# Kernel tuning notes

Hardware: AMD Instinct MI355X
Metric: run time of the kernel (lower is better)

## Reference

```python
import jax, jax.numpy as jnp
from jax import lax
import numpy as np

SEL = [46, 92]
A_SEL = [16, 32]
EPS = 1e-16


def _descriptors(xyz, atomtypes, box):
    # xyz: (B,N,3) float, atomtypes: (B,N) int, box: scalar
    B, N, _ = xyz.shape
    dm = xyz[:, :, None, :] - xyz[:, None, :, :] + EPS          # (B,N,N,3)
    dm = dm - box * jnp.round(dm / box)                          # min-image PBC
    dist = jnp.sqrt(jnp.sum(dm * dm, axis=-1))                   # (B,N,N)
    self_mask = jnp.eye(N, dtype=bool)[None]                     # exclude self
    radial, a_xyz_list, a_dist_list = [], [], []
    lf_d = lf_i = None
    for j, (selj, aselj) in enumerate(zip(SEL, A_SEL)):
        mask = (atomtypes == j)[:, None, :] & (~self_mask)       # (B,N,N)
        d_j = jnp.where(mask, dist, jnp.inf)
        k = max(selj, aselj, 2)
        neg, idx = lax.top_k(-d_j, k)                            # k smallest
        sd = -neg                                                # (B,N,k)
        if j == 0:
            lf_d, lf_i = sd[..., :2], idx[..., :2]
        else:
            better = sd[..., :2] < lf_d
            lf_d = jnp.where(better, sd[..., :2], lf_d)
            lf_i = jnp.where(better, idx[..., :2], lf_i)
        radial.append(1.0 / (sd[..., :selj] + EPS))
        a_xyz_list.append(jnp.take_along_axis(dm, idx[..., :aselj, None], axis=2))
        a_dist_list.append(sd[..., :aselj])
    a_xyz = jnp.concatenate(a_xyz_list, axis=2)                  # (B,N,sumA,3)
    a_dist = jnp.concatenate(a_dist_list, axis=2)[..., None]     # (B,N,sumA,1)
    # local frame from the 2 globally nearest neighbors
    l_xyz = jnp.take_along_axis(dm, lf_i[..., None], axis=2) / (lf_d[..., None] + EPS)
    r0, r1 = l_xyz[:, :, 0], l_xyz[:, :, 1]                      # (B,N,3)
    v2 = r1 - jnp.sum(r0 * r1, -1, keepdims=True) * r0
    v2 = v2 / jnp.linalg.norm(v2, axis=-1, keepdims=True)
    v3 = jnp.cross(r0, r1)
    v3 = v3 / jnp.linalg.norm(v3, axis=-1, keepdims=True)
    A = jnp.stack([r0, v2, v3], axis=-2)                         # (B,N,3,3)
    a_xyz = a_xyz / (a_dist + EPS)
    a_xyz = jnp.einsum('bnij,bnkj->bnki', A, a_xyz)
    a_xyz = a_xyz / (a_dist + EPS)  # faithful: source divides by a_dist twice
    return jnp.concatenate(radial + [a_xyz.reshape(B, N, -1)], axis=-1)


def _energy(xyz, atomtypes, box, params):
    # norm is (mean=0, std=1) in the source -> identity, skipped.
    desc = _descriptors(xyz, atomtypes, box)
    e = jnp.zeros(desc.shape[:2], desc.dtype)
    for t, layers in enumerate(params):
        h = desc
        for (W, b) in layers[:-1]:
            h = jnp.tanh(h @ W + b)
        W, b = layers[-1]
        e = jnp.where(atomtypes == t, (h @ W + b)[..., 0], e)
    return jnp.sum(e, axis=1)                                    # (B,)


def setup_inputs():
    key = jax.random.key(0)
    ks = jax.random.split(key, 16)
    B, N, box = 2, 2048, 27
    xyz = jax.random.uniform(ks[0], (B, N, 3), dtype=jnp.float32) * box
    atomtypes = jax.random.randint(ks[1], (B, N), 0, 2)
    D = sum(SEL) + 3 * sum(A_SEL)  # 282
    sizes = [D, 64, 64, 1]
    inp = {'xyz': xyz, 'atomtypes': atomtypes, 'box_size': box}
    ki = 2
    for t in range(2):
        for l in range(3):
            fi, fo = sizes[l], sizes[l + 1]
            inp[f'W{t}_{l}'] = jax.random.normal(ks[ki], (fi, fo), dtype=jnp.float32) / np.sqrt(fi).astype(np.float32)
            inp[f'b{t}_{l}'] = jnp.zeros((fo,), jnp.float32)
            ki += 1
    return inp


def reference(xyz, atomtypes, box_size, W0_0, b0_0, W0_1, b0_1, W0_2, b0_2,
              W1_0, b1_0, W1_1, b1_1, W1_2, b1_2):
    params = [[(W0_0, b0_0), (W0_1, b0_1), (W0_2, b0_2)],
              [(W1_0, b1_0), (W1_1, b1_1), (W1_2, b1_2)]]
    energy = _energy(xyz, atomtypes, box_size, params)
    forces = -jax.grad(lambda x: jnp.sum(_energy(x, atomtypes, box_size, params)))(xyz)
    return energy, forces
```

## Files before the change

kernel.cpp:

```cpp
#include <hip/hip_runtime.h>
#include <stdint.h>
#include <math.h>

#define BLOCK 256
#define WPB 4
#define SEL0 46
#define SEL1 92
#define ASEL0 16
#define ASEL1 32
#define NNB 138
#define NANG 48
#define DDIM 282
#define HID 64
#define FEPS 1e-16f
#define NPT 32
#define CAP 128
#define NMAX 2048
#define SFE (3*NMAX)
#define RGROUPS 8

__device__ __forceinline__ float mimg(float dx, float box, float ibox) {
    return dx - box * rintf(dx * ibox);
}

__device__ __forceinline__ void wsync() {
    asm volatile("s_waitcnt lgkmcnt(0)" ::: "memory");
    __builtin_amdgcn_wave_barrier();
}

__device__ __forceinline__ void decode(unsigned long long k, float& d, int& j) {
    uint32_t idx = (uint32_t)(k & 0xFFFFFFFFull);
    if (idx == 0xFFFFFFFFu) { d = 1e30f; j = -1; }
    else { d = __uint_as_float((uint32_t)(k >> 32)); j = (int)idx; }
}

__global__ __launch_bounds__(BLOCK)
void reduce_kernel(const float* __restrict__ rep, float* __restrict__ out,
                   int total, int B, int N, int sstride, int nspb, int rgs)
{
    int e = blockIdx.x * BLOCK + threadIdx.x;
    if (e >= total) return;
    int r0 = blockIdx.y * rgs;
    if (r0 >= nspb) return;
    int r1 = min(r0 + rgs, nspb);
    const float* p;
    if (e < B) {
        p = rep + (size_t)e * nspb * sstride + 3 * N;
    } else {
        int f = e - B;
        int b = f / (3 * N);
        int elem = f - b * 3 * N;
        p = rep + (size_t)b * nspb * sstride + elem;
    }
    p += (size_t)r0 * sstride;
    float s0=0,s1=0,s2=0,s3=0,s4=0,s5=0,s6=0,s7=0;
    int r = r0;
    const size_t st = (size_t)sstride;
    for (; r + 8 <= r1; r += 8) {
        s0 += p[0*st]; s1 += p[1*st]; s2 += p[2*st]; s3 += p[3*st];
        s4 += p[4*st]; s5 += p[5*st]; s6 += p[6*st]; s7 += p[7*st];
        p += 8*st;
    }
    float s = ((s0+s1)+(s2+s3)) + ((s4+s5)+(s6+s7));
    for (; r < r1; ++r) { s += *p; p += st; }
    atomicAdd(&out[e], s);
}

__global__ __launch_bounds__(BLOCK, 2)
void md_kernel(const float* __restrict__ xyz, const int* __restrict__ types,
               const void* __restrict__ boxp,
               const float* __restrict__ W0a, const float* __restrict__ B0a,
               const float* __restrict__ W1a, const float* __restrict__ B1a,
               const float* __restrict__ W2a, const float* __restrict__ B2a,
               const float* __restrict__ W0b, const float* __restrict__ B0b,
               const float* __restrict__ W1b, const float* __restrict__ B1b,
               const float* __restrict__ W2b, const float* __restrict__ B2b,
               float* __restrict__ out, float* __restrict__ slotbase,
               int sstride, int G, int B, int N)
{
    __shared__ unsigned long long A0s[WPB][CAP];
    __shared__ unsigned long long A1s[WPB][CAP];
    __shared__ float sdescs[WPB][DDIM];
    __shared__ float sgs[WPB][DDIM];
    __shared__ float sAs[WPB][9];
    __shared__ float sh1s[WPB][HID];
    __shared__ float sdh1s[WPB][HID];
    __shared__ float sF[3*NMAX + 8];

    const int w = threadIdx.x >> 6;
    const int lane = threadIdx.x & 63;
    const bool lmode = (slotbase != nullptr);

    for (int s2 = threadIdx.x; s2 <= SFE; s2 += BLOCK) sF[s2] = 0.0f;
    __syncthreads();

    unsigned long long* A0w = A0s[w];
    unsigned long long* A1w = A1s[w];
    float* sdescw = sdescs[w];
    float* sgw = sgs[w];
    float* sAw = sAs[w];
    float* sh1w = sh1s[w];
    float* sdh1w = sdh1s[w];

    int ib_test = ((const int*)boxp)[0];
    float box = (ib_test > 0 && ib_test < 1000000) ? (float)ib_test
                                                   : ((const float*)boxp)[0];
    float ibox = 1.0f / box;

    const int gpw = G / WPB;

    for (int k2 = 0; k2 < gpw; ++k2) {
      const int atom = blockIdx.x * G + w * gpw + k2;
      if (atom < B * N) {
        const int b = atom / N;
        const int i = atom - b * N;

        const float* X = xyz + (size_t)b * N * 3;
        const int*   T = types + (size_t)b * N;
        const int ti = T[i];
        const float xi = X[3*i+0], yi = X[3*i+1], zi = X[3*i+2];
        float* Fg = out + B + (size_t)3 * b * N;

        uint32_t rk[NPT];
        #pragma unroll
        for (int jj = 0; jj < NPT; ++jj) {
            int j = jj * 64 + lane;
            uint32_t k = 0x7FFFFFFFu;
            if (j < N && j != i) {
                float dx = mimg(xi - X[3*j+0], box, ibox);
                float dy = mimg(yi - X[3*j+1], box, ibox);
                float dz = mimg(zi - X[3*j+2], box, ibox);
                float d = sqrtf(dx*dx + dy*dy + dz*dz);
                k = __float_as_uint(d) | (T[j] ? 0x80000000u : 0u);
            }
            rk[jj] = k;
        }

        uint32_t t1 = 0;
        #pragma unroll
        for (int jj = 0; jj < NPT; ++jj) t1 += (rk[jj] >> 31);
        #pragma unroll
        for (int o = 32; o > 0; o >>= 1) t1 += __shfl_down(t1, o, 64);
        t1 = __shfl(t1, 0, 64);
        const int tot1 = (int)t1;
        const int tot0 = (N - 1) - tot1;
        const int need0 = min(SEL0, tot0);
        const int need1 = min(SEL1, tot1);

        const float vol = box * box * box;
        const float c43pi = 4.18879020f;
        float R0 = cbrtf(0.5f * (need0 + CAP) * vol / (c43pi * fmaxf((float)tot0, 1.0f)));
        float R1 = cbrtf(0.5f * (need1 + CAP) * vol / (c43pi * fmaxf((float)tot1, 1.0f)));
        uint32_t Rb0 = __float_as_uint(R0), Rb1 = __float_as_uint(R1);
        float lo0 = 0.0f, hi0 = -1.0f, lo1 = 0.0f, hi1 = -1.0f;
        for (int it = 0; it < 20; ++it) {
            uint32_t c0 = 0, c1 = 0;
            #pragma unroll
            for (int jj = 0; jj < NPT; ++jj) {
                uint32_t k = rk[jj];
                c0 += ((k < 0x80000000u) && (k < Rb0));
                c1 += ((k >= 0x80000000u) && ((k & 0x7FFFFFFFu) < Rb1));
            }
            uint32_t packed = c0 | (c1 << 16);
            #pragma unroll
            for (int o = 32; o > 0; o >>= 1) packed += __shfl_down(packed, o, 64);
            packed = __shfl(packed, 0, 64);
            int cc0 = (int)(packed & 0xFFFFu);
            int cc1 = (int)(packed >> 16);
            bool done0 = (cc0 >= need0 && cc0 <= CAP);
            bool done1 = (cc1 >= need1 && cc1 <= CAP);
            if (done0 && done1) break;
            if (!done0) {
                if (cc0 < need0) { lo0 = R0; R0 = (hi0 > 0.0f) ? 0.5f*(lo0+hi0) : R0*1.3f; }
                else             { hi0 = R0; R0 = 0.5f*(lo0+hi0); }
                Rb0 = __float_as_uint(R0);
            }
            if (!done1) {
                if (cc1 < need1) { lo1 = R1; R1 = (hi1 > 0.0f) ? 0.5f*(lo1+hi1) : R1*1.3f; }
                else             { hi1 = R1; R1 = 0.5f*(lo1+hi1); }
                Rb1 = __float_as_uint(R1);
            }
        }

        const unsigned long long lmlt = (1ull << lane) - 1ull;
        int base0 = 0, base1 = 0;
        #pragma unroll
        for (int jj = 0; jj < NPT; ++jj) {
            uint32_t k = rk[jj];
            bool p0 = (k < 0x80000000u) && (k < Rb0);
            bool p1 = (k >= 0x80000000u) && ((k & 0x7FFFFFFFu) < Rb1);
            unsigned long long m0 = __ballot(p0);
            unsigned long long m1 = __ballot(p1);
            if (p0) {
                int pos = base0 + __popcll(m0 & lmlt);
                if (pos < CAP)
                    A0w[pos] = ((unsigned long long)k << 32) | (uint32_t)(jj*64 + lane);
            }
            if (p1) {
                int pos = base1 + __popcll(m1 & lmlt);
                if (pos < CAP)
                    A1w[pos] = ((unsigned long long)(k & 0x7FFFFFFFu) << 32) | (uint32_t)(jj*64 + lane);
            }
            base0 += __popcll(m0);
            base1 += __popcll(m1);
        }
        const int c0n = min(base0, CAP);
        const int c1n = min(base1, CAP);
        #pragma unroll
        for (int t = lane; t < CAP; t += 64) {
            if (t >= c0n) A0w[t] = ~0ull;
            if (t >= c1n) A1w[t] = ~0ull;
        }
        wsync();

        {
            unsigned long long va = A0w[lane], vb = A0w[lane + 64];
            unsigned long long wa = A1w[lane], wb = A1w[lane + 64];
            #pragma unroll
            for (int size = 2; size <= 128; size <<= 1) {
                #pragma unroll
                for (int stride = 64; stride > 0; stride >>= 1) {
                    if (stride >= size) continue;
                    if (stride == 64) {
                        unsigned long long mn = va < vb ? va : vb;
                        unsigned long long mx = va < vb ? vb : va;
                        va = mn; vb = mx;
                        mn = wa < wb ? wa : wb;
                        mx = wa < wb ? wb : wa;
                        wa = mn; wb = mx;
                    } else {
                        bool keep_lo = (lane & stride) == 0;
                        bool asc0 = ((lane & size) == 0);
                        bool asc1 = (((lane + 64) & size) == 0);
                        unsigned long long oa = __shfl_xor(va, stride, 64);
                        unsigned long long ob = __shfl_xor(vb, stride, 64);
                        va = (asc0 == keep_lo) ? (va < oa ? va : oa) : (va > oa ? va : oa);
                        vb = (asc1 == keep_lo) ? (vb < ob ? vb : ob) : (vb > ob ? vb : ob);
                        oa = __shfl_xor(wa, stride, 64);
                        ob = __shfl_xor(wb, stride, 64);
                        wa = (asc0 == keep_lo) ? (wa < oa ? wa : oa) : (wa > oa ? wa : oa);
                        wb = (asc1 == keep_lo) ? (wb < ob ? wb : ob) : (wb > ob ? wb : ob);
                    }
                }
            }
            A0w[lane] = va; A0w[lane + 64] = vb;
            A1w[lane] = wa; A1w[lane + 64] = wb;
        }
        wsync();

        for (int t = lane; t < NNB; t += 64) {
            unsigned long long k = (t < SEL0) ? A0w[t] : A1w[t - SEL0];
            float d; int j; decode(k, d, j);
            sdescw[t] = 1.0f / (d + FEPS);
        }

        float f_ld0 = 1.0f, f_ld1 = 1.0f; int f_j0 = -1, f_j1 = -1;
        float r0x=0,r0y=0,r0z=0, r1x=0,r1y=0,r1z=0;
        float u0x=0,u0y=0,u0z=0, u1x=0,u1y=0,u1z=0;
        float f_s=0, f_n2=1, f_n3=1;
        float e2x=0,e2y=0,e2z=0, e3x=0,e3y=0,e3z=0;
        if (lane == 0) {
            float da0, da1, db0, db1; int ja0, ja1, jb0, jb1;
            decode(A0w[0], da0, ja0);
            decode(A0w[1], da1, ja1);
            decode(A1w[0], db0, jb0);
            decode(A1w[1], db1, jb1);
            f_ld0 = (db0 < da0) ? db0 : da0;  f_j0 = (db0 < da0) ? jb0 : ja0;
            f_ld1 = (db1 < da1) ? db1 : da1;  f_j1 = (db1 < da1) ? jb1 : ja1;
            if (f_j0 < 0) f_j0 = i;
            if (f_j1 < 0) f_j1 = i;
            u0x = mimg(xi - X[3*f_j0+0], box, ibox);
            u0y = mimg(yi - X[3*f_j0+1], box, ibox);
            u0z = mimg(zi - X[3*f_j0+2], box, ibox);
            u1x = mimg(xi - X[3*f_j1+0], box, ibox);
            u1y = mimg(yi - X[3*f_j1+1], box, ibox);
            u1z = mimg(zi - X[3*f_j1+2], box, ibox);
            float id0 = 1.0f/(f_ld0 + FEPS), id1 = 1.0f/(f_ld1 + FEPS);
            r0x = u0x*id0; r0y = u0y*id0; r0z = u0z*id0;
            r1x = u1x*id1; r1y = u1y*id1; r1z = u1z*id1;
            f_s = r0x*r1x + r0y*r1y + r0z*r1z;
            float v2x = r1x - f_s*r0x, v2y = r1y - f_s*r0y, v2z = r1z - f_s*r0z;
            f_n2 = sqrtf(v2x*v2x + v2y*v2y + v2z*v2z);
            e2x = v2x/f_n2; e2y = v2y/f_n2; e2z = v2z/f_n2;
            float cx = r0y*r1z - r0z*r1y;
            float cy = r0z*r1x - r0x*r1z;
            float cz = r0x*r1y - r0y*r1x;
            f_n3 = sqrtf(cx*cx + cy*cy + cz*cz);
            e3x = cx/f_n3; e3y = cy/f_n3; e3z = cz/f_n3;
            sAw[0]=r0x; sAw[1]=r0y; sAw[2]=r0z;
            sAw[3]=e2x; sAw[4]=e2y; sAw[5]=e2z;
            sAw[6]=e3x; sAw[7]=e3y; sAw[8]=e3z;
        }
        wsync();

        if (lane < NANG) {
            int slot = (lane < ASEL0) ? lane : SEL0 + (lane - ASEL0);
            unsigned long long k = (slot < SEL0) ? A0w[slot] : A1w[slot - SEL0];
            float d; int j; decode(k, d, j);
            float dx = 0, dy = 0, dz = 0;
            if (j >= 0) {
                dx = mimg(xi - X[3*j+0], box, ibox);
                dy = mimg(yi - X[3*j+1], box, ibox);
                dz = mimg(zi - X[3*j+2], box, ibox);
            }
            float de = d + FEPS;
            float q = 1.0f/(de*de);
            float wx = sAw[0]*dx + sAw[1]*dy + sAw[2]*dz;
            float wy = sAw[3]*dx + sAw[4]*dy + sAw[5]*dz;
            float wz = sAw[6]*dx + sAw[7]*dy + sAw[8]*dz;
            sdescw[NNB + 3*lane + 0] = wx*q;
            sdescw[NNB + 3*lane + 1] = wy*q;
            sdescw[NNB + 3*lane + 2] = wz*q;
        }
        wsync();

        const float* W0 = ti ? W0b : W0a;  const float* B0 = ti ? B0b : B0a;
        const float* W1 = ti ? W1b : W1a;  const float* B1 = ti ? B1b : B1a;
        const float* W2 = ti ? W2b : W2a;  const float* B2 = ti ? B2b : B2a;

        float a0 = 0.0f, a1 = 0.0f, a2 = 0.0f, a3 = 0.0f;
        for (int d = 0; d < DDIM - 2; d += 4) {
            a0 = fmaf(sdescw[d+0], W0[(d+0)*HID + lane], a0);
            a1 = fmaf(sdescw[d+1], W0[(d+1)*HID + lane], a1);
            a2 = fmaf(sdescw[d+2], W0[(d+2)*HID + lane], a2);
            a3 = fmaf(sdescw[d+3], W0[(d+3)*HID + lane], a3);
        }
        a0 = fmaf(sdescw[DDIM-2], W0[(DDIM-2)*HID + lane], a0);
        a1 = fmaf(sdescw[DDIM-1], W0[(DDIM-1)*HID + lane], a1);
        float h1 = tanhf(B0[lane] + ((a0 + a1) + (a2 + a3)));
        sh1w[lane] = h1;
        wsync();

        float acc2 = B1[lane];
        #pragma unroll
        for (int m = 0; m < HID; ++m) acc2 = fmaf(sh1w[m], W1[m*HID + lane], acc2);
        float h2 = tanhf(acc2);
        float w2v = W2[lane];
        float part = h2 * w2v;
        #pragma unroll
        for (int o = 32; o > 0; o >>= 1) part += __shfl_down(part, o, 64);
        if (lane == 0) {
            if (lmode) atomicAdd(&sF[SFE], part + B2[0]);
            else       atomicAdd(&out[b], part + B2[0]);
        }
        float dh2 = (1.0f - h2*h2) * w2v;
        sdh1w[lane] = dh2;
        wsync();

        float accb = 0.0f;
        #pragma unroll
        for (int m = 0; m < HID; ++m) accb = fmaf(W1[lane*HID + m], sdh1w[m], accb);
        wsync();
        float dh1 = (1.0f - h1*h1) * accb;
        sdh1w[lane] = dh1;
        wsync();

        for (int d = lane; d < DDIM; d += 64) {
            float a = 0.0f;
            #pragma unroll
            for (int m = 0; m < HID; ++m) a = fmaf(W0[d*HID + m], sdh1w[m], a);
            sgw[d] = a;
        }
        wsync();

        float rG[9];
        #pragma unroll
        for (int q9 = 0; q9 < 9; ++q9) rG[q9] = 0.0f;
        float fix = 0.0f, fiy = 0.0f, fiz = 0.0f;

        for (int t = lane; t < NNB; t += 64) {
            unsigned long long k = (t < SEL0) ? A0w[t] : A1w[t - SEL0];
            float d; int j; decode(k, d, j);
            if (j >= 0) {
                float dx = mimg(xi - X[3*j+0], box, ibox);
                float dy = mimg(yi - X[3*j+1], box, ibox);
                float dz = mimg(zi - X[3*j+2], box, ibox);
                float gr = sgw[t];
                float de = d + FEPS;
                float coef = -gr / (d * de * de);
                float gx = coef*dx, gy = coef*dy, gz = coef*dz;
                int a = -1;
                if (t < ASEL0) a = t;
                else if (t >= SEL0 && t < SEL0 + ASEL1) a = ASEL0 + (t - SEL0);
                if (a >= 0) {
                    float q = 1.0f/(de*de);
                    float gax = sgw[NNB+3*a+0], gay = sgw[NNB+3*a+1], gaz = sgw[NNB+3*a+2];
                    float wx = sAw[0]*dx + sAw[1]*dy + sAw[2]*dz;
                    float wy = sAw[3]*dx + sAw[4]*dy + sAw[5]*dz;
                    float wz = sAw[6]*dx + sAw[7]*dy + sAw[8]*dz;
                    float tx = sAw[0]*gax + sAw[3]*gay + sAw[6]*gaz;
                    float ty = sAw[1]*gax + sAw[4]*gay + sAw[7]*gaz;
                    float tz = sAw[2]*gax + sAw[5]*gay + sAw[8]*gaz;
                    float gw = gax*wx + gay*wy + gaz*wz;
                    float c2 = -2.0f * gw * q / (de * d);
                    gx += q*tx + c2*dx;
                    gy += q*ty + c2*dy;
                    gz += q*tz + c2*dz;
                    rG[0] += gax*dx*q; rG[1] += gax*dy*q; rG[2] += gax*dz*q;
                    rG[3] += gay*dx*q; rG[4] += gay*dy*q; rG[5] += gay*dz*q;
                    rG[6] += gaz*dx*q; rG[7] += gaz*dy*q; rG[8] += gaz*dz*q;
                }
                if (lmode) {
                    atomicAdd(&sF[3*j+0], gx);
                    atomicAdd(&sF[3*j+1], gy);
                    atomicAdd(&sF[3*j+2], gz);
                } else {
                    atomicAdd(&Fg[3*j+0], gx);
                    atomicAdd(&Fg[3*j+1], gy);
                    atomicAdd(&Fg[3*j+2], gz);
                }
                fix -= gx; fiy -= gy; fiz -= gz;
            }
        }

        #pragma unroll
        for (int o = 32; o > 0; o >>= 1) {
            #pragma unroll
            for (int q9 = 0; q9 < 9; ++q9) rG[q9] += __shfl_down(rG[q9], o, 64);
            fix += __shfl_down(fix, o, 64);
            fiy += __shfl_down(fiy, o, 64);
            fiz += __shfl_down(fiz, o, 64);
        }

        if (lane == 0) {
            float g0x=rG[0], g0y=rG[1], g0z=rG[2];
            float g2x=rG[3], g2y=rG[4], g2z=rG[5];
            float g3x=rG[6], g3y=rG[7], g3z=rG[8];
            float d3 = g3x*e3x + g3y*e3y + g3z*e3z;
            float in3 = 1.0f/f_n3;
            float dcx = (g3x - d3*e3x)*in3;
            float dcy = (g3y - d3*e3y)*in3;
            float dcz = (g3z - d3*e3z)*in3;
            float gr0x = r1y*dcz - r1z*dcy;
            float gr0y = r1z*dcx - r1x*dcz;
            float gr0z = r1x*dcy - r1y*dcx;
            float gr1x = dcy*r0z - dcz*r0y;
            float gr1y = dcz*r0x - dcx*r0z;
            float gr1z = dcx*r0y - dcy*r0x;
            float d2 = g2x*e2x + g2y*e2y + g2z*e2z;
            float in2 = 1.0f/f_n2;
            float dvx = (g2x - d2*e2x)*in2;
            float dvy = (g2y - d2*e2y)*in2;
            float dvz = (g2z - d2*e2z)*in2;
            gr1x += dvx; gr1y += dvy; gr1z += dvz;
            gr0x -= f_s*dvx; gr0y -= f_s*dvy; gr0z -= f_s*dvz;
            float dss = -(dvx*r0x + dvy*r0y + dvz*r0z);
            gr0x += dss*r1x; gr0y += dss*r1y; gr0z += dss*r1z;
            gr1x += dss*r0x; gr1y += dss*r0y; gr1z += dss*r0z;
            gr0x += g0x; gr0y += g0y; gr0z += g0z;
            float de0 = f_ld0 + FEPS;
            float dot0 = gr0x*u0x + gr0y*u0y + gr0z*u0z;
            float k0 = dot0 / (f_ld0 * de0 * de0);
            float gu0x = gr0x/de0 - k0*u0x;
            float gu0y = gr0y/de0 - k0*u0y;
            float gu0z = gr0z/de0 - k0*u0z;
            float de1 = f_ld1 + FEPS;
            float dot1 = gr1x*u1x + gr1y*u1y + gr1z*u1z;
            float k1 = dot1 / (f_ld1 * de1 * de1);
            float gu1x = gr1x/de1 - k1*u1x;
            float gu1y = gr1y/de1 - k1*u1y;
            float gu1z = gr1z/de1 - k1*u1z;
            fix -= gu0x + gu1x;
            fiy -= gu0y + gu1y;
            fiz -= gu0z + gu1z;
            if (lmode) {
                atomicAdd(&sF[3*f_j0+0], gu0x); atomicAdd(&sF[3*f_j0+1], gu0y); atomicAdd(&sF[3*f_j0+2], gu0z);
                atomicAdd(&sF[3*f_j1+0], gu1x); atomicAdd(&sF[3*f_j1+1], gu1y); atomicAdd(&sF[3*f_j1+2], gu1z);
                atomicAdd(&sF[3*i+0], fix);     atomicAdd(&sF[3*i+1], fiy);     atomicAdd(&sF[3*i+2], fiz);
            } else {
                atomicAdd(&Fg[3*f_j0+0], gu0x); atomicAdd(&Fg[3*f_j0+1], gu0y); atomicAdd(&Fg[3*f_j0+2], gu0z);
                atomicAdd(&Fg[3*f_j1+0], gu1x); atomicAdd(&Fg[3*f_j1+1], gu1y); atomicAdd(&Fg[3*f_j1+2], gu1z);
                atomicAdd(&Fg[3*i+0], fix);     atomicAdd(&Fg[3*i+1], fiy);     atomicAdd(&Fg[3*i+2], fiz);
            }
        }
      }
    }

    __syncthreads();
    if (lmode) {
        float* slotp = slotbase + (size_t)blockIdx.x * sstride;
        for (int s2 = threadIdx.x; s2 < 3*N; s2 += BLOCK) slotp[s2] = sF[s2];
        if (threadIdx.x == 0) slotp[3*N] = sF[SFE];
    }
}

extern "C" void kernel_launch(void* const* d_in, const int* in_sizes, int n_in,
                              void* d_out, int out_size, void* d_ws, size_t ws_size,
                              hipStream_t stream) {
    const float* xyz  = (const float*)d_in[0];
    const int*   types = (const int*)d_in[1];
    const void*  boxp = d_in[2];
    int BN = in_sizes[1];
    int B = out_size - 3*BN;
    if (B < 1) B = 1;
    int N = BN / B;

    int sstride = 3 * N + 32;
    int G = 0;
    if (N <= NMAX) {
        for (int g = 8; g <= 64; g <<= 1) {
            if (N % g || BN % g) continue;
            size_t needb = (size_t)(BN / g) * sstride * sizeof(float);
            if (needb <= ws_size) { G = g; break; }
        }
    }

    if (G) {
        float* rep = (float*)d_ws;
        int nblk = BN / G;
        hipMemsetAsync(d_out, 0, (size_t)out_size * sizeof(float), stream);
        md_kernel<<<dim3(nblk), dim3(BLOCK), 0, stream>>>(
            xyz, types, boxp,
            (const float*)d_in[3],  (const float*)d_in[4],
            (const float*)d_in[5],  (const float*)d_in[6],
            (const float*)d_in[7],  (const float*)d_in[8],
            (const float*)d_in[9],  (const float*)d_in[10],
            (const float*)d_in[11], (const float*)d_in[12],
            (const float*)d_in[13], (const float*)d_in[14],
            (float*)d_out, rep, sstride, G, B, N);
        int nspb = N / G;
        int ngroups = (nspb < RGROUPS) ? nspb : RGROUPS;
        int rgs = (nspb + ngroups - 1) / ngroups;
        int nb = (out_size + BLOCK - 1) / BLOCK;
        reduce_kernel<<<dim3(nb, ngroups), dim3(BLOCK), 0, stream>>>(
            rep, (float*)d_out, out_size, B, N, sstride, nspb, rgs);
    } else {
        hipMemsetAsync(d_out, 0, (size_t)out_size * sizeof(float), stream);
        int nblk = (BN + WPB - 1) / WPB;
        md_kernel<<<dim3(nblk), dim3(BLOCK), 0, stream>>>(
            xyz, types, boxp,
            (const float*)d_in[3],  (const float*)d_in[4],
            (const float*)d_in[5],  (const float*)d_in[6],
            (const float*)d_in[7],  (const float*)d_in[8],
            (const float*)d_in[9],  (const float*)d_in[10],
            (const float*)d_in[11], (const float*)d_in[12],
            (const float*)d_in[13], (const float*)d_in[14],
            (float*)d_out, nullptr, 0, WPB, B, N);
    }
}
```

Before: 240.7 us.

## Use one atom per wave with 8-wave blocks and fuse radius search with compaction

Drops the multiple-atoms-per-wave loop. Each block now runs 8 waves with one atom each, so there are far more blocks, and launch bounds ask for 4 blocks per CU. The radius bisection loop now compacts candidates into shared memory on every iteration, which removes the separate count reduction and the final compaction pass, and the type count uses ballot+popcount. The trade-off is that each block's private force buffer (sF, about 24 KB) now covers only 8 atoms, so the workspace grows and the reduction kernel has more partial slots to sum. Shared memory per block also grows, which may limit how many blocks fit on a CU.

```diff
diff --git a/kernel.cpp b/kernel.cpp
--- a/kernel.cpp
+++ b/kernel.cpp
@@ -2,8 +2,8 @@
 #include <stdint.h>
 #include <math.h>
 
-#define BLOCK 256
-#define WPB 4
+#define BLOCK 512
+#define WPB 8
 #define SEL0 46
 #define SEL1 92
 #define ASEL0 16
@@ -34,11 +34,11 @@
     else { d = __uint_as_float((uint32_t)(k >> 32)); j = (int)idx; }
 }
 
-__global__ __launch_bounds__(BLOCK)
+__global__ __launch_bounds__(256)
 void reduce_kernel(const float* __restrict__ rep, float* __restrict__ out,
                    int total, int B, int N, int sstride, int nspb, int rgs)
 {
-    int e = blockIdx.x * BLOCK + threadIdx.x;
+    int e = blockIdx.x * 256 + threadIdx.x;
     if (e >= total) return;
     int r0 = blockIdx.y * rgs;
     if (r0 >= nspb) return;
@@ -66,7 +66,7 @@
     atomicAdd(&out[e], s);
 }
 
-__global__ __launch_bounds__(BLOCK, 2)
+__global__ __launch_bounds__(BLOCK, 4)
 void md_kernel(const float* __restrict__ xyz, const int* __restrict__ types,
                const void* __restrict__ boxp,
                const float* __restrict__ W0a, const float* __restrict__ B0a,
@@ -76,7 +76,7 @@
                const float* __restrict__ W1b, const float* __restrict__ B1b,
                const float* __restrict__ W2b, const float* __restrict__ B2b,
                float* __restrict__ out, float* __restrict__ slotbase,
-               int sstride, int G, int B, int N)
+               int sstride, int B, int N)
 {
     __shared__ unsigned long long A0s[WPB][CAP];
     __shared__ unsigned long long A1s[WPB][CAP];
@@ -94,26 +94,23 @@
     for (int s2 = threadIdx.x; s2 <= SFE; s2 += BLOCK) sF[s2] = 0.0f;
     __syncthreads();
 
-    unsigned long long* A0w = A0s[w];
-    unsigned long long* A1w = A1s[w];
-    float* sdescw = sdescs[w];
-    float* sgw = sgs[w];
-    float* sAw = sAs[w];
-    float* sh1w = sh1s[w];
-    float* sdh1w = sdh1s[w];
-
-    int ib_test = ((const int*)boxp)[0];
-    float box = (ib_test > 0 && ib_test < 1000000) ? (float)ib_test
-                                                   : ((const float*)boxp)[0];
-    float ibox = 1.0f / box;
-
-    const int gpw = G / WPB;
-
-    for (int k2 = 0; k2 < gpw; ++k2) {
-      const int atom = blockIdx.x * G + w * gpw + k2;
-      if (atom < B * N) {
+    const int atom = blockIdx.x * WPB + w;
+    if (atom < B * N) {
+        unsigned long long* A0w = A0s[w];
+        unsigned long long* A1w = A1s[w];
+        float* sdescw = sdescs[w];
+        float* sgw = sgs[w];
+        float* sAw = sAs[w];
+        float* sh1w = sh1s[w];
+        float* sdh1w = sdh1s[w];
+
         const int b = atom / N;
         const int i = atom - b * N;
+
+        int ib_test = ((const int*)boxp)[0];
+        float box = (ib_test > 0 && ib_test < 1000000) ? (float)ib_test
+                                                       : ((const float*)boxp)[0];
+        float ibox = 1.0f / box;
 
         const float* X = xyz + (size_t)b * N * 3;
         const int*   T = types + (size_t)b * N;
@@ -138,10 +135,8 @@
 
         uint32_t t1 = 0;
         #pragma unroll
-        for (int jj = 0; jj < NPT; ++jj) t1 += (rk[jj] >> 31);
-        #pragma unroll
-        for (int o = 32; o > 0; o >>= 1) t1 += __shfl_down(t1, o, 64);
-        t1 = __shfl(t1, 0, 64);
+        for (int jj = 0; jj < NPT; ++jj)
+            t1 += (uint32_t)__popcll(__ballot((rk[jj] >> 31) != 0u));
         const int tot1 = (int)t1;
         const int tot0 = (N - 1) - tot1;
         const int need0 = min(SEL0, tot0);
@@ -151,61 +146,46 @@
         const float c43pi = 4.18879020f;
         float R0 = cbrtf(0.5f * (need0 + CAP) * vol / (c43pi * fmaxf((float)tot0, 1.0f)));
         float R1 = cbrtf(0.5f * (need1 + CAP) * vol / (c43pi * fmaxf((float)tot1, 1.0f)));
-        uint32_t Rb0 = __float_as_uint(R0), Rb1 = __float_as_uint(R1);
         float lo0 = 0.0f, hi0 = -1.0f, lo1 = 0.0f, hi1 = -1.0f;
+        const unsigned long long lmlt = (1ull << lane) - 1ull;
+        int c0n = 0, c1n = 0;
         for (int it = 0; it < 20; ++it) {
-            uint32_t c0 = 0, c1 = 0;
+            uint32_t Rb0 = __float_as_uint(R0), Rb1 = __float_as_uint(R1);
+            int base0 = 0, base1 = 0;
             #pragma unroll
             for (int jj = 0; jj < NPT; ++jj) {
                 uint32_t k = rk[jj];
-                c0 += ((k < 0x80000000u) && (k < Rb0));
-                c1 += ((k >= 0x80000000u) && ((k & 0x7FFFFFFFu) < Rb1));
-            }
-            uint32_t packed = c0 | (c1 << 16);
-            #pragma unroll
-            for (int o = 32; o > 0; o >>= 1) packed += __shfl_down(packed, o, 64);
-            packed = __shfl(packed, 0, 64);
-            int cc0 = (int)(packed & 0xFFFFu);
-            int cc1 = (int)(packed >> 16);
-            bool done0 = (cc0 >= need0 && cc0 <= CAP);
-            bool done1 = (cc1 >= need1 && cc1 <= CAP);
-            if (done0 && done1) break;
-            if (!done0) {
-                if (cc0 < need0) { lo0 = R0; R0 = (hi0 > 0.0f) ? 0.5f*(lo0+hi0) : R0*1.3f; }
-                else             { hi0 = R0; R0 = 0.5f*(lo0+hi0); }
-                Rb0 = __float_as_uint(R0);
-            }
-            if (!done1) {
-                if (cc1 < need1) { lo1 = R1; R1 = (hi1 > 0.0f) ? 0.5f*(lo1+hi1) : R1*1.3f; }
-                else             { hi1 = R1; R1 = 0.5f*(lo1+hi1); }
-                Rb1 = __float_as_uint(R1);
-            }
-        }
-
-        const unsigned long long lmlt = (1ull << lane) - 1ull;
-        int base0 = 0, base1 = 0;
-        #pragma unroll
-        for (int jj = 0; jj < NPT; ++jj) {
-            uint32_t k = rk[jj];
-            bool p0 = (k < 0x80000000u) && (k < Rb0);
-            bool p1 = (k >= 0x80000000u) && ((k & 0x7FFFFFFFu) < Rb1);
-            unsigned long long m0 = __ballot(p0);
-            unsigned long long m1 = __ballot(p1);
-            if (p0) {
-                int pos = base0 + __popcll(m0 & lmlt);
-                if (pos < CAP)
-                    A0w[pos] = ((unsigned long long)k << 32) | (uint32_t)(jj*64 + lane);
-            }
-            if (p1) {
-                int pos = base1 + __popcll(m1 & lmlt);
-                if (pos < CAP)
-                    A1w[pos] = ((unsigned long long)(k & 0x7FFFFFFFu) << 32) | (uint32_t)(jj*64 + lane);
-            }
-            base0 += __popcll(m0);
-            base1 += __popcll(m1);
-        }
-        const int c0n = min(base0, CAP);
-        const int c1n = min(base1, CAP);
+                bool p0 = (k < 0x80000000u) && (k < Rb0);
+                bool p1 = (k >= 0x80000000u) && ((k & 0x7FFFFFFFu) < Rb1);
+                unsigned long long m0 = __ballot(p0);
+                unsigned long long m1 = __ballot(p1);
+                if (p0) {
+                    int pos = base0 + __popcll(m0 & lmlt);
+                    if (pos < CAP)
+                        A0w[pos] = ((unsigned long long)k << 32) | (uint32_t)(jj*64 + lane);
+                }
+                if (p1) {
+                    int pos = base1 + __popcll(m1 & lmlt);
+                    if (pos < CAP)
+                        A1w[pos] = ((unsigned long long)(k & 0x7FFFFFFFu) << 32) | (uint32_t)(jj*64 + lane);
+                }
+                base0 += __popcll(m0);
+                base1 += __popcll(m1);
+            }
+            bool ok0 = (base0 >= need0 && base0 <= CAP);
+            bool ok1 = (base1 >= need1 && base1 <= CAP);
+            c0n = min(base0, CAP);
+            c1n = min(base1, CAP);
+            if (ok0 && ok1) break;
+            if (!ok0) {
+                if (base0 < need0) { lo0 = R0; R0 = (hi0 > 0.0f) ? 0.5f*(lo0+hi0) : R0*1.3f; }
+                else               { hi0 = R0; R0 = 0.5f*(lo0+hi0); }
+            }
+            if (!ok1) {
+                if (base1 < need1) { lo1 = R1; R1 = (hi1 > 0.0f) ? 0.5f*(lo1+hi1) : R1*1.3f; }
+                else               { hi1 = R1; R1 = 0.5f*(lo1+hi1); }
+            }
+        }
         #pragma unroll
         for (int t = lane; t < CAP; t += 64) {
             if (t >= c0n) A0w[t] = ~0ull;
@@ -473,7 +453,6 @@
                 atomicAdd(&Fg[3*i+0], fix);     atomicAdd(&Fg[3*i+1], fiy);     atomicAdd(&Fg[3*i+2], fiz);
             }
         }
-      }
     }
 
     __syncthreads();
@@ -496,19 +475,14 @@
     int N = BN / B;
 
     int sstride = 3 * N + 32;
-    int G = 0;
-    if (N <= NMAX) {
-        for (int g = 8; g <= 64; g <<= 1) {
-            if (N % g || BN % g) continue;
-            size_t needb = (size_t)(BN / g) * sstride * sizeof(float);
-            if (needb <= ws_size) { G = g; break; }
-        }
-    }
-
-    if (G) {
+    bool ok = (N <= NMAX) && (N % WPB == 0) && (BN % WPB == 0) &&
+              ((size_t)(BN / WPB) * sstride * sizeof(float) <= ws_size);
+
+    hipMemsetAsync(d_out, 0, (size_t)out_size * sizeof(float), stream);
+
+    if (ok) {
         float* rep = (float*)d_ws;
-        int nblk = BN / G;
-        hipMemsetAsync(d_out, 0, (size_t)out_size * sizeof(float), stream);
+        int nblk = BN / WPB;
         md_kernel<<<dim3(nblk), dim3(BLOCK), 0, stream>>>(
             xyz, types, boxp,
             (const float*)d_in[3],  (const float*)d_in[4],
@@ -517,15 +491,14 @@
             (const float*)d_in[9],  (const float*)d_in[10],
             (const float*)d_in[11], (const float*)d_in[12],
             (const float*)d_in[13], (const float*)d_in[14],
-            (float*)d_out, rep, sstride, G, B, N);
-        int nspb = N / G;
+            (float*)d_out, rep, sstride, B, N);
+        int nspb = N / WPB;
         int ngroups = (nspb < RGROUPS) ? nspb : RGROUPS;
         int rgs = (nspb + ngroups - 1) / ngroups;
-        int nb = (out_size + BLOCK - 1) / BLOCK;
-        reduce_kernel<<<dim3(nb, ngroups), dim3(BLOCK), 0, stream>>>(
+        int nb = (out_size + 255) / 256;
+        reduce_kernel<<<dim3(nb, ngroups), dim3(256), 0, stream>>>(
             rep, (float*)d_out, out_size, B, N, sstride, nspb, rgs);
     } else {
-        hipMemsetAsync(d_out, 0, (size_t)out_size * sizeof(float), stream);
         int nblk = (BN + WPB - 1) / WPB;
         md_kernel<<<dim3(nblk), dim3(BLOCK), 0, stream>>>(
             xyz, types, boxp,
@@ -535,6 +508,6 @@
             (const float*)d_in[9],  (const float*)d_in[10],
             (const float*)d_in[11], (const float*)d_in[12],
             (const float*)d_in[13], (const float*)d_in[14],
-            (float*)d_out, nullptr, 0, WPB, B, N);
+            (float*)d_out, nullptr, 0, B, N);
     }
 }
```

After: 228.1 us, median of 2. -5.2%, faster.
